# Kernel optimization log

Measured on AMD Instinct MI355X. Metric: run time of the kernel, lower is better.

Reference implementation:

```python
import jax, jax.numpy as jnp
import numpy as np

NEG_SLOPE = 0.2


def gat_layer(x, src, dst, W, att_src, att_dst, bias, n_nodes):
    # PyG GATConv (heads=1): h = x @ W; per-edge logit = LeakyReLU(a_src.h[src] + a_dst.h[dst]);
    # softmax over edges grouped by destination node; out[d] = sum alpha * h[src] + bias.
    h = x @ W                                  # [N, F]
    a_s = h @ att_src                          # [N]
    a_d = h @ att_dst                          # [N]
    e = a_s[src] + a_d[dst]                    # [E]
    e = jnp.where(e > 0, e, NEG_SLOPE * e)     # leaky_relu
    m = jax.ops.segment_max(e, dst, num_segments=n_nodes)   # [N]
    w = jnp.exp(e - m[dst])                    # [E]
    z = jax.ops.segment_sum(w, dst, num_segments=n_nodes)   # [N]
    alpha = w / z[dst]                         # [E] (self-loops guarantee z>0)
    out = jax.ops.segment_sum(alpha[:, None] * h[src], dst, num_segments=n_nodes)
    return out + bias


def setup_inputs() -> dict:
    key = jax.random.key(0)
    ks = jax.random.split(key, 10)
    N, E, C_IN, H1, H2 = 100000, 3200000, 128, 50, 40
    x = jax.random.normal(ks[0], (N, C_IN), dtype=jnp.float32)
    edge_index = jax.random.randint(ks[1], (2, E), 0, N, dtype=jnp.int64)
    g1 = 1.0 / np.sqrt(C_IN)
    g2 = 1.0 / np.sqrt(H1)
    return {
        "x": x,
        "edge_index": edge_index,
        "W1": jax.random.normal(ks[2], (C_IN, H1), dtype=jnp.float32) * g1,
        "att_src1": jax.random.normal(ks[3], (H1,), dtype=jnp.float32) * g2,
        "att_dst1": jax.random.normal(ks[4], (H1,), dtype=jnp.float32) * g2,
        "bias1": jnp.zeros((H1,), dtype=jnp.float32),
        "W2": jax.random.normal(ks[5], (H1, H2), dtype=jnp.float32) * g2,
        "att_src2": jax.random.normal(ks[6], (H2,), dtype=jnp.float32) / np.sqrt(H2),
        "att_dst2": jax.random.normal(ks[7], (H2,), dtype=jnp.float32) / np.sqrt(H2),
        "bias2": jnp.zeros((H2,), dtype=jnp.float32),
    }


def reference(x, edge_index, W1, att_src1, att_dst1, bias1, W2, att_src2, att_dst2, bias2):
    n_nodes = x.shape[0]
    # PyG GATConv default add_self_loops=True: append (i, i) for every node.
    loop = jnp.arange(n_nodes, dtype=edge_index.dtype)
    src = jnp.concatenate([edge_index[0], loop])
    dst = jnp.concatenate([edge_index[1], loop])
    h = jax.nn.relu(gat_layer(x, src, dst, W1, att_src1, att_dst1, bias1, n_nodes))
    h = jax.nn.relu(gat_layer(h, src, dst, W2, att_src2, att_dst2, bias2, n_nodes))
    return h, edge_index
```

## Files before the change

### kernel.cpp

```cpp
#include <hip/hip_runtime.h>
#include <hip/hip_bf16.h>
#include <math.h>

#define NEG_SLOPE 0.2f
#define RBITS 9
#define RNODES 512
#define CHUNK 16384
#define CAP   18432
#define HS    32


__device__ __forceinline__ float waveReduceSum(float v) {
    #pragma unroll
    for (int off = 32; off > 0; off >>= 1) v += __shfl_xor(v, off);
    return v;
}

__device__ __forceinline__ unsigned pack_bf16(float a, float b) {
    __hip_bfloat162 p(__float2bfloat16(a), __float2bfloat16(b));
    return *reinterpret_cast<unsigned*>(&p);
}
__device__ __forceinline__ float bf16lo_f(unsigned u) { return __uint_as_float(u << 16); }
__device__ __forceinline__ float bf16hi_f(unsigned u) { return __uint_as_float(u & 0xFFFF0000u); }


__global__ void zero_small(int* __restrict__ p, int n) {
    int i = blockIdx.x * blockDim.x + threadIdx.x;
    if (i < n) p[i] = 0;
}

__global__ void binning(const int* __restrict__ src, const int* __restrict__ dst,
                        int* __restrict__ bcursor, int* __restrict__ binned,
                        long E, int N, long TOT) {
    __shared__ int hist[256];
    __shared__ int base[256];
    int t = threadIdx.x;
    if (t < 256) hist[t] = 0;
    __syncthreads();
    long c0 = blockIdx.x * (long)CHUNK;
    long c1 = c0 + CHUNK; if (c1 > TOT) c1 = TOT;
    for (long i = c0 + t; i < c1; i += 256) {
        int d = (i < E) ? dst[i] : (int)(i - E);
        atomicAdd(&hist[d >> RBITS], 1);
    }
    __syncthreads();
    if (t < 256) {
        int c = hist[t];
        base[t] = c ? atomicAdd(&bcursor[t], c) : 0;
        hist[t] = 0;
    }
    __syncthreads();
    for (long i = c0 + t; i < c1; i += 256) {
        int s, d;
        if (i < E) { s = src[i]; d = dst[i]; } else { s = d = (int)(i - E); }
        int b = d >> RBITS;
        int p = base[b] + atomicAdd(&hist[b], 1);
        if (p >= CAP) p = CAP - 1;
        binned[(long)b * CAP + p] = ((d & (RNODES - 1)) << 17) | s;
    }
}

__global__ void bucket_scan(const int* __restrict__ bcursor, int* __restrict__ bstarts,
                            int* __restrict__ starts, int NB, int N, int TOT) {
    __shared__ int s[256];
    int t = threadIdx.x;
    int v = (t < NB) ? bcursor[t] : 0;
    s[t] = v;
    __syncthreads();
    for (int off = 1; off < 256; off <<= 1) {
        int u = (t >= off) ? s[t - off] : 0;
        __syncthreads();
        s[t] += u;
        __syncthreads();
    }
    int excl = s[t] - v;
    if (t < NB) bstarts[t] = excl;
    if (t == 0) { bstarts[NB] = TOT; starts[N] = TOT; }
}

__global__ void bucket_csr(const int* __restrict__ binned, const int* __restrict__ bstarts,
                           int* __restrict__ starts, int* __restrict__ csr_src, int N) {
    __shared__ int cnt[RNODES];
    __shared__ int scn[RNODES];
    int b = blockIdx.x, t = threadIdx.x;
    int node0 = b << RBITS;
    int R = N - node0; if (R > RNODES) R = RNODES;
    int e0 = bstarts[b];
    int ecnt = bstarts[b + 1] - e0;
    const int* bin = binned + (long)b * CAP;
    cnt[t] = 0;
    __syncthreads();
    for (int i = t; i < ecnt; i += RNODES)
        atomicAdd(&cnt[bin[i] >> 17], 1);
    __syncthreads();
    int v = cnt[t];
    scn[t] = v;
    __syncthreads();
    for (int off = 1; off < RNODES; off <<= 1) {
        int u = (t >= off) ? scn[t - off] : 0;
        __syncthreads();
        scn[t] += u;
        __syncthreads();
    }
    int excl = scn[t] - v;
    if (t < R) starts[node0 + t] = e0 + excl;
    __syncthreads();
    cnt[t] = excl;
    __syncthreads();
    for (int i = t; i < ecnt; i += RNODES) {
        int packed = bin[i];
        int ld = packed >> 17;
        int p = atomicAdd(&cnt[ld], 1);
        csr_src[e0 + p] = packed & 0x1FFFF;
    }
}

__global__ void transposeW(const float* __restrict__ W, float* __restrict__ WT,
                           int K, int F, int KP, int FP) {
    int i = blockIdx.x * blockDim.x + threadIdx.x;
    if (i >= FP * KP) return;
    int f = i / KP, k = i - f * KP;
    WT[i] = (f < F && k < K) ? W[k * F + f] : 0.f;
}

template <int K, int KP, int F>
__global__ __launch_bounds__(512) void gemm_tile(
        const float* __restrict__ x, const float* __restrict__ WT,
        const float* __restrict__ att_s, const float* __restrict__ att_d,
        unsigned* __restrict__ hb, float* __restrict__ as_, float* __restrict__ ad_,
        int N) {
    constexpr int PF = F / 2;
    __shared__ float xT[KP * 65];
    __shared__ float asl[64], adl[64];
    int t = threadIdx.x;
    int lane = t & 63;
    int w = t >> 6;
    long n0 = (long)blockIdx.x * 64;
    int n = (int)n0 + lane;

    if (t < 64) { asl[t] = 0.f; adl[t] = 0.f; }
    for (int idx = t; idx < KP * 64; idx += 512) {
        int nn = idx / KP, k = idx - nn * KP;
        float v = 0.f;
        if (k < K && n0 + nn < N) v = x[(n0 + nn) * (long)K + k];
        xT[k * 65 + nn] = v;
    }
    __syncthreads();

    int f0 = __builtin_amdgcn_readfirstlane(w * 8);
    float acc[8] = {0.f, 0.f, 0.f, 0.f, 0.f, 0.f, 0.f, 0.f};
    if (f0 < F) {
        const float* wbase = WT + (long)f0 * KP;
        for (int k0 = 0; k0 < KP; k0 += 4) {
            float x0 = xT[(k0 + 0) * 65 + lane];
            float x1 = xT[(k0 + 1) * 65 + lane];
            float x2 = xT[(k0 + 2) * 65 + lane];
            float x3 = xT[(k0 + 3) * 65 + lane];
            #pragma unroll
            for (int j = 0; j < 8; ++j) {
                const float* wr = wbase + j * KP + k0;
                float a = acc[j];
                a = fmaf(wr[0], x0, a);
                a = fmaf(wr[1], x1, a);
                a = fmaf(wr[2], x2, a);
                a = fmaf(wr[3], x3, a);
                acc[j] = a;
            }
        }
        float ps = 0.f, pd = 0.f;
        #pragma unroll
        for (int j = 0; j < 8; ++j) {
            float sa = (f0 + j < F) ? att_s[f0 + j] : 0.f;
            float da = (f0 + j < F) ? att_d[f0 + j] : 0.f;
            ps = fmaf(acc[j], sa, ps);
            pd = fmaf(acc[j], da, pd);
        }
        atomicAdd(&asl[lane], ps);
        atomicAdd(&adl[lane], pd);
    }
    __syncthreads();

    if (f0 < F && n < N) {
        int f0h = f0 >> 1;
        #pragma unroll
        for (int q = 0; q < 4; ++q) {
            int fp = f0h + q;
            if (fp < PF) hb[(long)n * HS + fp] = pack_bf16(acc[2 * q], acc[2 * q + 1]);
        }
    }
    if (w == 0 && n < N) { as_[n] = asl[lane]; ad_[n] = adl[lane]; }
}

template <int F>
__global__ void gat_gather(const int* __restrict__ csr_src, const int* __restrict__ starts,
                           const float* __restrict__ as_, const float* __restrict__ ad_,
                           const unsigned* __restrict__ hb, const float* __restrict__ bias,
                           float* __restrict__ out, int N) {
    constexpr int PF = F / 2;
    int lane = threadIdx.x & 63;
    int half = lane >> 5;
    int flane = lane & 31;
    bool actf = (flane < PF);
    long wave = (blockIdx.x * (long)blockDim.x + threadIdx.x) >> 6;
    if (wave >= N) return;
    int d = (int)wave;
    int s0 = starts[d], s1 = starts[d + 1];
    float add = ad_[d];

    float lsum = 0.f;
    float acc0 = 0.f, acc1 = 0.f;
    for (int base = s0; base < s1; base += 64) {
        int k = base + lane;
        float w = 0.f; int s = 0;
        if (k < s1) {
            s = csr_src[k];
            float e = as_[s] + add;
            e = e > 0.f ? e : NEG_SLOPE * e;
            w = __expf(e);
        }
        lsum += w;
        int cnt = min(64, s1 - base);
        int pairs = (cnt + 1) >> 1;
        for (int j = 0; j < pairs; j += 4) {
            #pragma unroll
            for (int u = 0; u < 4; ++u) {
                int idx = 2 * (j + u) + half;
                float wp = __shfl(w, idx);
                int   sp = __shfl(s, idx);
                unsigned hv = 0;
                if (actf) hv = hb[(long)sp * HS + flane];
                acc0 = fmaf(wp, bf16lo_f(hv), acc0);
                acc1 = fmaf(wp, bf16hi_f(hv), acc1);
            }
        }
    }
    acc0 += __shfl_xor(acc0, 32);
    acc1 += __shfl_xor(acc1, 32);
    float l = waveReduceSum(lsum);

    if (lane < PF) {
        float inv = 1.f / l;
        float v0 = acc0 * inv + bias[2 * lane];
        float v1 = acc1 * inv + bias[2 * lane + 1];
        v0 = v0 > 0.f ? v0 : 0.f;
        v1 = v1 > 0.f ? v1 : 0.f;
        ((float2*)(out + (long)d * F))[lane] = make_float2(v0, v1);
    }
}

__global__ void copy_edges4(const int4* __restrict__ ei, float4* __restrict__ out, long n4) {
    long i = blockIdx.x * (long)blockDim.x + threadIdx.x;
    if (i < n4) {
        int4 v = ei[i];
        out[i] = make_float4((float)v.x, (float)v.y, (float)v.z, (float)v.w);
    }
}
__global__ void copy_edges_tail(const int* __restrict__ ei, float* __restrict__ out,
                                long lo, long n) {
    long i = lo + blockIdx.x * (long)blockDim.x + threadIdx.x;
    if (i < n) out[i] = (float)ei[i];
}


extern "C" void kernel_launch(void* const* d_in, const int* in_sizes, int n_in,
                              void* d_out, int out_size, void* d_ws, size_t ws_size,
                              hipStream_t stream) {
    const float* x         = (const float*)d_in[0];
    const int*   edge_idx  = (const int*)d_in[1];
    const float* W1        = (const float*)d_in[2];
    const float* att_src1  = (const float*)d_in[3];
    const float* att_dst1  = (const float*)d_in[4];
    const float* bias1     = (const float*)d_in[5];
    const float* W2        = (const float*)d_in[6];
    const float* att_src2  = (const float*)d_in[7];
    const float* att_dst2  = (const float*)d_in[8];
    const float* bias2     = (const float*)d_in[9];

    const int  CIN = 128, F1 = 50, F2 = 40;
    const int  KP1 = 128, FP1 = 56;
    const int  KP2 = 52,  FP2 = 40;
    const int  N = in_sizes[0] / CIN;
    const long E = in_sizes[1] / 2;
    const int* src = edge_idx;
    const int* dst = edge_idx + E;
    const long TOT = E + N;
    const int  NB = (N + RNODES - 1) >> RBITS;

    char* wsb = (char*)d_ws;
    size_t regionA = (size_t)NB * CAP * 4;
    if ((size_t)N * HS * 4 > regionA) regionA = (size_t)N * HS * 4;
    int*      binned = (int*)wsb;
    unsigned* hb     = (unsigned*)wsb;
    float*    hout   = (float*)(wsb + regionA);
    float*    as_    = hout + (long)N * F1;
    float*    ad_    = as_ + N;
    int*      starts  = (int*)(ad_ + N);
    int*      csr_src = starts + (N + 1);
    int*      bstarts = csr_src + TOT;
    int*      bcursor = bstarts + (NB + 1);
    float*    WT1     = (float*)(bcursor + NB + 3);
    float*    WT2     = WT1 + FP1 * KP1;

    float* out_h = (float*)d_out;
    float* out_e = out_h + (long)N * F2;

    const int B = 256;
    const int nodeWaveBlocks = (N + 3) / 4;
    const int nTileBlocks = (N + 63) / 64;
    const int nBinBlocks = (int)((TOT + CHUNK - 1) / CHUNK);

    transposeW<<<dim3((FP1 * KP1 + 255) / 256), dim3(256), 0, stream>>>(W1, WT1, CIN, F1, KP1, FP1);
    transposeW<<<dim3((FP2 * KP2 + 255) / 256), dim3(256), 0, stream>>>(W2, WT2, F1, F2, KP2, FP2);
    zero_small<<<dim3(1), dim3(256), 0, stream>>>(bcursor, NB);
    binning<<<dim3(nBinBlocks), dim3(B), 0, stream>>>(src, dst, bcursor, binned, E, N, TOT);
    bucket_scan<<<dim3(1), dim3(256), 0, stream>>>(bcursor, bstarts, starts, NB, N, (int)TOT);
    bucket_csr<<<dim3(NB), dim3(RNODES), 0, stream>>>(binned, bstarts, starts, csr_src, N);

    gemm_tile<CIN, KP1, F1><<<dim3(nTileBlocks), dim3(512), 0, stream>>>(x, WT1, att_src1, att_dst1, hb, as_, ad_, N);
    gat_gather<F1><<<dim3(nodeWaveBlocks), dim3(B), 0, stream>>>(csr_src, starts, as_, ad_, hb, bias1, hout, N);

    gemm_tile<F1, KP2, F2><<<dim3(nTileBlocks), dim3(512), 0, stream>>>(hout, WT2, att_src2, att_dst2, hb, as_, ad_, N);
    gat_gather<F2><<<dim3(nodeWaveBlocks), dim3(B), 0, stream>>>(csr_src, starts, as_, ad_, hb, bias2, out_h, N);

    long n_e = 2 * E;
    long n4  = n_e / 4;
    copy_edges4<<<dim3((int)((n4 + B - 1) / B)), dim3(B), 0, stream>>>((const int4*)edge_idx, (float4*)out_e, n4);
    if (n_e - n4 * 4 > 0)
        copy_edges_tail<<<dim3(1), dim3(B), 0, stream>>>(edge_idx, out_e, n4 * 4, n_e);
}
```

Baseline: 443.2 us.

## Gather four edges per wave step with 8-byte loads; widen bucket_csr blocks

The gather kernel now splits each wave into four 16-lane groups. Each lane loads a uint2, which is four bf16 features, so one step processes four edges instead of two, and partial sums are combined with xor shuffles at the end. gemm_tile now writes padded feature pairs (FP/2) so the wider loads read zero-padded values rather than stale data. bucket_csr launches 1024 threads per block to process bucket edges with more parallelism. The aim is fewer load instructions and more edges in flight per iteration. The cost is more reduction shuffles, and lanes 13-15 of each group sit idle for F=50.

Result: slower. 462.8 us (+4.4%).

```diff
diff --git a/kernel.cpp b/kernel.cpp
--- a/kernel.cpp
+++ b/kernel.cpp
@@ -78,8 +78,9 @@
     if (t == 0) { bstarts[NB] = TOT; starts[N] = TOT; }
 }
 
-__global__ void bucket_csr(const int* __restrict__ binned, const int* __restrict__ bstarts,
-                           int* __restrict__ starts, int* __restrict__ csr_src, int N) {
+__global__ __launch_bounds__(1024) void bucket_csr(
+        const int* __restrict__ binned, const int* __restrict__ bstarts,
+        int* __restrict__ starts, int* __restrict__ csr_src, int N) {
     __shared__ int cnt[RNODES];
     __shared__ int scn[RNODES];
     int b = blockIdx.x, t = threadIdx.x;
@@ -88,26 +89,27 @@
     int e0 = bstarts[b];
     int ecnt = bstarts[b + 1] - e0;
     const int* bin = binned + (long)b * CAP;
-    cnt[t] = 0;
-    __syncthreads();
-    for (int i = t; i < ecnt; i += RNODES)
+    if (t < RNODES) cnt[t] = 0;
+    __syncthreads();
+    for (int i = t; i < ecnt; i += 1024)
         atomicAdd(&cnt[bin[i] >> 17], 1);
     __syncthreads();
-    int v = cnt[t];
-    scn[t] = v;
+    int v = (t < RNODES) ? cnt[t] : 0;
+    if (t < RNODES) scn[t] = v;
     __syncthreads();
     for (int off = 1; off < RNODES; off <<= 1) {
-        int u = (t >= off) ? scn[t - off] : 0;
+        int u = (t >= off && t < RNODES) ? scn[t - off] : 0;
         __syncthreads();
-        scn[t] += u;
+        if (t < RNODES) scn[t] += u;
         __syncthreads();
     }
-    int excl = scn[t] - v;
-    if (t < R) starts[node0 + t] = e0 + excl;
-    __syncthreads();
-    cnt[t] = excl;
-    __syncthreads();
-    for (int i = t; i < ecnt; i += RNODES) {
+    if (t < RNODES) {
+        int excl = scn[t] - v;
+        if (t < R) starts[node0 + t] = e0 + excl;
+        cnt[t] = excl;
+    }
+    __syncthreads();
+    for (int i = t; i < ecnt; i += 1024) {
         int packed = bin[i];
         int ld = packed >> 17;
         int p = atomicAdd(&cnt[ld], 1);
@@ -123,13 +125,12 @@
     WT[i] = (f < F && k < K) ? W[k * F + f] : 0.f;
 }
 
-template <int K, int KP, int F>
+template <int K, int KP, int F, int FPH>
 __global__ __launch_bounds__(512) void gemm_tile(
         const float* __restrict__ x, const float* __restrict__ WT,
         const float* __restrict__ att_s, const float* __restrict__ att_d,
         unsigned* __restrict__ hb, float* __restrict__ as_, float* __restrict__ ad_,
         int N) {
-    constexpr int PF = F / 2;
     __shared__ float xT[KP * 65];
     __shared__ float asl[64], adl[64];
     int t = threadIdx.x;
@@ -185,7 +186,7 @@
         #pragma unroll
         for (int q = 0; q < 4; ++q) {
             int fp = f0h + q;
-            if (fp < PF) hb[(long)n * HS + fp] = pack_bf16(acc[2 * q], acc[2 * q + 1]);
+            if (fp < FPH) hb[(long)n * HS + fp] = pack_bf16(acc[2 * q], acc[2 * q + 1]);
         }
     }
     if (w == 0 && n < N) { as_[n] = asl[lane]; ad_[n] = adl[lane]; }
@@ -196,11 +197,11 @@
                            const float* __restrict__ as_, const float* __restrict__ ad_,
                            const unsigned* __restrict__ hb, const float* __restrict__ bias,
                            float* __restrict__ out, int N) {
-    constexpr int PF = F / 2;
+    constexpr int PFU = (F / 2 + 1) >> 1;
     int lane = threadIdx.x & 63;
-    int half = lane >> 5;
-    int flane = lane & 31;
-    bool actf = (flane < PF);
+    int q = lane >> 4;
+    int fl = lane & 15;
+    bool actf = (fl < PFU);
     long wave = (blockIdx.x * (long)blockDim.x + threadIdx.x) >> 6;
     if (wave >= N) return;
     int d = (int)wave;
@@ -208,7 +209,7 @@
     float add = ad_[d];
 
     float lsum = 0.f;
-    float acc0 = 0.f, acc1 = 0.f;
+    float a0 = 0.f, a1 = 0.f, a2 = 0.f, a3 = 0.f;
     for (int base = s0; base < s1; base += 64) {
         int k = base + lane;
         float w = 0.f; int s = 0;
@@ -220,31 +221,46 @@
         }
         lsum += w;
         int cnt = min(64, s1 - base);
-        int pairs = (cnt + 1) >> 1;
-        for (int j = 0; j < pairs; j += 4) {
-            #pragma unroll
-            for (int u = 0; u < 4; ++u) {
-                int idx = 2 * (j + u) + half;
-                float wp = __shfl(w, idx);
-                int   sp = __shfl(s, idx);
-                unsigned hv = 0;
-                if (actf) hv = hb[(long)sp * HS + flane];
-                acc0 = fmaf(wp, bf16lo_f(hv), acc0);
-                acc1 = fmaf(wp, bf16hi_f(hv), acc1);
+        int quads = (cnt + 3) >> 2;
+        #pragma unroll 2
+        for (int j = 0; j < quads; ++j) {
+            int idx = 4 * j + q;
+            float wp = __shfl(w, idx);
+            int   sp = __shfl(s, idx);
+            if (actf) {
+                uint2 hv = *(const uint2*)(hb + (long)sp * HS + 2 * fl);
+                a0 = fmaf(wp, bf16lo_f(hv.x), a0);
+                a1 = fmaf(wp, bf16hi_f(hv.x), a1);
+                a2 = fmaf(wp, bf16lo_f(hv.y), a2);
+                a3 = fmaf(wp, bf16hi_f(hv.y), a3);
             }
         }
     }
-    acc0 += __shfl_xor(acc0, 32);
-    acc1 += __shfl_xor(acc1, 32);
+    #pragma unroll
+    for (int off = 16; off < 64; off <<= 1) {
+        a0 += __shfl_xor(a0, off);
+        a1 += __shfl_xor(a1, off);
+        a2 += __shfl_xor(a2, off);
+        a3 += __shfl_xor(a3, off);
+    }
     float l = waveReduceSum(lsum);
 
-    if (lane < PF) {
+    if (actf) {
         float inv = 1.f / l;
-        float v0 = acc0 * inv + bias[2 * lane];
-        float v1 = acc1 * inv + bias[2 * lane + 1];
+        int fb = 4 * fl;
+        float v0 = a0 * inv + bias[fb];
+        float v1 = a1 * inv + bias[fb + 1];
         v0 = v0 > 0.f ? v0 : 0.f;
         v1 = v1 > 0.f ? v1 : 0.f;
-        ((float2*)(out + (long)d * F))[lane] = make_float2(v0, v1);
+        float2* orow = (float2*)(out + (long)d * F);
+        orow[2 * fl] = make_float2(v0, v1);
+        if (fb + 2 < F) {
+            float v2 = a2 * inv + bias[fb + 2];
+            float v3 = a3 * inv + bias[fb + 3];
+            v2 = v2 > 0.f ? v2 : 0.f;
+            v3 = v3 > 0.f ? v3 : 0.f;
+            orow[2 * fl + 1] = make_float2(v2, v3);
+        }
     }
 }
 
@@ -314,12 +330,12 @@
     zero_small<<<dim3(1), dim3(256), 0, stream>>>(bcursor, NB);
     binning<<<dim3(nBinBlocks), dim3(B), 0, stream>>>(src, dst, bcursor, binned, E, N, TOT);
     bucket_scan<<<dim3(1), dim3(256), 0, stream>>>(bcursor, bstarts, starts, NB, N, (int)TOT);
-    bucket_csr<<<dim3(NB), dim3(RNODES), 0, stream>>>(binned, bstarts, starts, csr_src, N);
-
-    gemm_tile<CIN, KP1, F1><<<dim3(nTileBlocks), dim3(512), 0, stream>>>(x, WT1, att_src1, att_dst1, hb, as_, ad_, N);
+    bucket_csr<<<dim3(NB), dim3(1024), 0, stream>>>(binned, bstarts, starts, csr_src, N);
+
+    gemm_tile<CIN, KP1, F1, FP1 / 2><<<dim3(nTileBlocks), dim3(512), 0, stream>>>(x, WT1, att_src1, att_dst1, hb, as_, ad_, N);
     gat_gather<F1><<<dim3(nodeWaveBlocks), dim3(B), 0, stream>>>(csr_src, starts, as_, ad_, hb, bias1, hout, N);
 
-    gemm_tile<F1, KP2, F2><<<dim3(nTileBlocks), dim3(512), 0, stream>>>(hout, WT2, att_src2, att_dst2, hb, as_, ad_, N);
+    gemm_tile<F1, KP2, F2, FP2 / 2><<<dim3(nTileBlocks), dim3(512), 0, stream>>>(hout, WT2, att_src2, att_dst2, hb, as_, ad_, N);
     gat_gather<F2><<<dim3(nodeWaveBlocks), dim3(B), 0, stream>>>(csr_src, starts, as_, ad_, hb, bias2, out_h, N);
 
     long n_e = 2 * E;
```
